# Kernel optimization log

Hardware: AMD Instinct MI355X
Metric: run time of the kernel (lower is better)

The kernel has to match this reference:

```python
import jax, jax.numpy as jnp
import numpy as np

N_NODES = 100000
N_EDGES = 1600000
IN_CH = 128
OUT_CH = 128


def setup_inputs() -> dict:
    key = jax.random.key(0)
    k1, k2, k3 = jax.random.split(key, 3)
    x = jax.random.normal(k1, (N_NODES, IN_CH), dtype=jnp.float32)
    edge_index = jax.random.randint(k2, (2, N_EDGES), 0, N_NODES, dtype=jnp.int64)
    # Glorot-style init like PyG GCNConv
    W = jax.random.normal(k3, (IN_CH, OUT_CH), dtype=jnp.float32) * (1.0 / np.sqrt(IN_CH))
    b = jnp.zeros((OUT_CH,), dtype=jnp.float32)
    return {"x": x, "edge_index": edge_index, "W": W, "b": b}


def reference(x, edge_index, W, b):
    N = x.shape[0]
    # add self-loops (PyG GCNConv default add_self_loops=True)
    loop = jnp.arange(N, dtype=edge_index.dtype)
    src = jnp.concatenate([edge_index[0], loop])
    dst = jnp.concatenate([edge_index[1], loop])
    # symmetric normalization: deg computed over destination (col)
    deg = jax.ops.segment_sum(jnp.ones_like(src, dtype=x.dtype), dst, num_segments=N)
    dinv = jnp.where(deg > 0, jax.lax.rsqrt(deg), 0.0)
    norm = dinv[src] * dinv[dst]  # [E+N]
    xw = x @ W  # [N, out_ch]
    msg = xw[src] * norm[:, None]  # gather + scale, [E+N, out_ch]
    out = jax.ops.segment_sum(msg, dst, num_segments=N) + b  # scatter-add
    return jax.nn.relu(out)
```

## Files before the change

### kernel.cpp

```cpp
#include <hip/hip_runtime.h>
#include <hip/hip_bf16.h>

constexpr int CH    = 128;
constexpr int BSH   = 7;
constexpr int CAPSH = 12;

typedef __attribute__((ext_vector_type(8))) short short8v;
typedef __attribute__((ext_vector_type(4))) float f32x4;

__device__ __forceinline__ unsigned short f2bf(float f) {
    unsigned u = __float_as_uint(f);
    u = (u + 0x7fffu + ((u >> 16) & 1u)) >> 16;
    return (unsigned short)u;
}

__global__ __launch_bounds__(256) void k_bin(const int* __restrict__ src,
                                             const int* __restrict__ dst, int E,
                                             int* __restrict__ bucket_cnt,
                                             unsigned* __restrict__ packed,
                                             const float* __restrict__ W,
                                             unsigned short* __restrict__ Wt,
                                             int nbuck) {
    __shared__ int hist[1024];
    int t = threadIdx.x;
    if (blockIdx.x < 32) {
        int idx = blockIdx.x * 256 + t;
        int c  = idx & 127;
        int k2 = (idx >> 7) * 2;
        unsigned pk = (unsigned)f2bf(W[(size_t)k2 * CH + c]) |
                      ((unsigned)f2bf(W[(size_t)(k2 + 1) * CH + c]) << 16);
        *(unsigned*)(Wt + (size_t)c * CH + k2) = pk;
    }
    for (int i = t; i < nbuck; i += 256) hist[i] = 0;
    __syncthreads();
    int chunk = (E + gridDim.x - 1) / gridDim.x;
    int e0 = blockIdx.x * chunk;
    int e1 = min(e0 + chunk, E);
    for (int e = e0 + t; e < e1; e += 256)
        atomicAdd(&hist[dst[e] >> BSH], 1);
    __syncthreads();
    for (int i = t; i < nbuck; i += 256) {
        int h = hist[i];
        hist[i] = (h > 0) ? atomicAdd(&bucket_cnt[i], h) : 0;
    }
    __syncthreads();
    for (int e = e0 + t; e < e1; e += 256) {
        int d = dst[e];
        int bkt = d >> BSH;
        int pos = atomicAdd(&hist[bkt], 1);
        packed[((size_t)bkt << CAPSH) + pos] =
            (unsigned)src[e] | ((unsigned)(d & ((1 << BSH) - 1)) << 20);
    }
}

__global__ __launch_bounds__(256) void k_bucket(const int* __restrict__ bucket_cnt,
                                                const unsigned* __restrict__ packed,
                                                int* __restrict__ eidx,
                                                uint2* __restrict__ rowinfo,
                                                float* __restrict__ dinv, int N) {
    __shared__ int fh[128];
    __shared__ int fs[128];
    __shared__ int fc[128];
    int b = blockIdx.x;
    int t = threadIdx.x;
    int cnt = bucket_cnt[b];
    if (t < 128) fh[t] = 0;
    __syncthreads();
    const unsigned* pk = packed + ((size_t)b << CAPSH);
    for (int i = t; i < cnt; i += 256)
        atomicAdd(&fh[(pk[i] >> 20) & 127], 1);
    __syncthreads();
    if (t < 128) fs[t] = fh[t];
    __syncthreads();
    for (int off = 1; off < 128; off <<= 1) {
        int v = 0;
        if (t < 128 && t >= off) v = fs[t - off];
        __syncthreads();
        if (t < 128) fs[t] += v;
        __syncthreads();
    }
    if (t < 128) {
        int excl = fs[t] - fh[t];
        fc[t] = excl;
        int node = (b << BSH) + t;
        if (node < N) {
            rowinfo[node] = make_uint2((unsigned)((b << CAPSH) + excl), (unsigned)fh[t]);
            dinv[node] = rsqrtf((float)fh[t] + 1.0f);
        }
    }
    __syncthreads();
    int* eo = eidx + ((size_t)b << CAPSH);
    for (int i = t; i < cnt; i += 256) {
        unsigned p = pk[i];
        int f = (p >> 20) & 127;
        int pos = atomicAdd(&fc[f], 1);
        eo[pos] = (int)(p & 0xFFFFF);
    }
}

__global__ __launch_bounds__(256) void k_gemm(const float* __restrict__ x,
                                              const unsigned short* __restrict__ Wt,
                                              const float* __restrict__ dinv,
                                              unsigned short* __restrict__ xwb, int N) {
    __shared__ __align__(16) unsigned short xs[64 * CH];
    int t = threadIdx.x;
    int w = t >> 6, lane = t & 63;
    int c16 = lane & 15, kq = lane >> 4, kb = kq * 8;
    int row0 = blockIdx.x * 64;
    int arow = row0 + w * 16 + c16;
    bool av = arow < N;
    const float* xp = x + (size_t)(av ? arow : 0) * CH;

    f32x4 acc[8];
    #pragma unroll
    for (int f = 0; f < 8; ++f) acc[f] = (f32x4){0.f, 0.f, 0.f, 0.f};

    #pragma unroll
    for (int kc = 0; kc < 4; ++kc) {
        float4 x0 = make_float4(0.f, 0.f, 0.f, 0.f), x1 = x0;
        if (av) {
            x0 = ((const float4*)(xp + kc * 32 + kb))[0];
            x1 = ((const float4*)(xp + kc * 32 + kb))[1];
        }
        union { short8v v; __hip_bfloat162 h[4]; } au;
        au.h[0] = __float22bfloat162_rn(make_float2(x0.x, x0.y));
        au.h[1] = __float22bfloat162_rn(make_float2(x0.z, x0.w));
        au.h[2] = __float22bfloat162_rn(make_float2(x1.x, x1.y));
        au.h[3] = __float22bfloat162_rn(make_float2(x1.z, x1.w));
        #pragma unroll
        for (int f = 0; f < 8; ++f) {
            short8v b = *(const short8v*)(Wt + (size_t)(f * 16 + c16) * CH + kc * 32 + kb);
            acc[f] = __builtin_amdgcn_mfma_f32_16x16x32_bf16(au.v, b, acc[f], 0, 0, 0);
        }
    }

    #pragma unroll
    for (int r = 0; r < 4; ++r) {
        int row_l = w * 16 + kq * 4 + r;
        int grow  = row0 + row_l;
        float dv  = (grow < N) ? dinv[grow] : 0.f;
        #pragma unroll
        for (int f = 0; f < 8; ++f) {
            int col = f * 16 + c16;
            unsigned bo = ((unsigned)((row_l * CH + col) * 2)) ^ ((unsigned)(row_l & 7) << 4);
            *(unsigned short*)((char*)xs + bo) = f2bf(acc[f][r] * dv);
        }
    }
    __syncthreads();
    #pragma unroll
    for (int i = 0; i < 4; ++i) {
        int g = i * 256 + t;
        int row_l = g >> 4;
        unsigned bo = ((unsigned)(g * 16)) ^ ((unsigned)(row_l & 7) << 4);
        uint4 v = *(const uint4*)((const char*)xs + bo);
        int row = row0 + row_l;
        if (row < N) ((uint4*)(xwb + (size_t)row * CH))[g & 15] = v;
    }
}

__global__ __launch_bounds__(256) void k_gather(const uint2* __restrict__ rowinfo,
                                                const int* __restrict__ eidx,
                                                const unsigned short* __restrict__ xwb,
                                                const float* __restrict__ dinv,
                                                const float* __restrict__ bias,
                                                float* __restrict__ out, int N) {
    int n = blockIdx.x * 4 + (threadIdx.x >> 6);
    if (n >= N) return;
    int lane = threadIdx.x & 63;
    int q    = lane >> 4;
    int c16  = lane & 15;
    uint2 ri = rowinfo[n];
    int beg = (int)ri.x;
    int deg = (int)ri.y;
    float acc[8];
    #pragma unroll
    for (int i = 0; i < 8; ++i) acc[i] = 0.f;

    for (int p0 = 0; p0 < deg; p0 += 64) {
        int m = deg - p0; if (m > 64) m = 64;
        int myi = 0;
        if (lane < m) myi = eidx[beg + p0 + lane];
        for (int j = 0; j < m; j += 4) {
            int jj = j + q;
            int ss = __shfl(myi, jj & 63);
            int s  = (jj < m) ? ss : N;
            uint4 u = ((const uint4*)(xwb + (size_t)s * CH))[c16];
            acc[0] += __uint_as_float(u.x << 16);
            acc[1] += __uint_as_float(u.x & 0xffff0000u);
            acc[2] += __uint_as_float(u.y << 16);
            acc[3] += __uint_as_float(u.y & 0xffff0000u);
            acc[4] += __uint_as_float(u.z << 16);
            acc[5] += __uint_as_float(u.z & 0xffff0000u);
            acc[6] += __uint_as_float(u.w << 16);
            acc[7] += __uint_as_float(u.w & 0xffff0000u);
        }
    }
    #pragma unroll
    for (int i = 0; i < 8; ++i) {
        acc[i] += __shfl_xor(acc[i], 16);
        acc[i] += __shfl_xor(acc[i], 32);
    }
    if (lane < 16) {
        float dn = dinv[n];
        uint4 u = ((const uint4*)(xwb + (size_t)n * CH))[c16];
        acc[0] += __uint_as_float(u.x << 16);
        acc[1] += __uint_as_float(u.x & 0xffff0000u);
        acc[2] += __uint_as_float(u.y << 16);
        acc[3] += __uint_as_float(u.y & 0xffff0000u);
        acc[4] += __uint_as_float(u.z << 16);
        acc[5] += __uint_as_float(u.z & 0xffff0000u);
        acc[6] += __uint_as_float(u.w << 16);
        acc[7] += __uint_as_float(u.w & 0xffff0000u);
        float4 b0 = ((const float4*)bias)[c16 * 2];
        float4 b1 = ((const float4*)bias)[c16 * 2 + 1];
        float4 o0, o1;
        o0.x = fmaxf(fmaf(acc[0], dn, b0.x), 0.f);
        o0.y = fmaxf(fmaf(acc[1], dn, b0.y), 0.f);
        o0.z = fmaxf(fmaf(acc[2], dn, b0.z), 0.f);
        o0.w = fmaxf(fmaf(acc[3], dn, b0.w), 0.f);
        o1.x = fmaxf(fmaf(acc[4], dn, b1.x), 0.f);
        o1.y = fmaxf(fmaf(acc[5], dn, b1.y), 0.f);
        o1.z = fmaxf(fmaf(acc[6], dn, b1.z), 0.f);
        o1.w = fmaxf(fmaf(acc[7], dn, b1.w), 0.f);
        ((float4*)(out + (size_t)n * CH))[c16 * 2]     = o0;
        ((float4*)(out + (size_t)n * CH))[c16 * 2 + 1] = o1;
    }
}

extern "C" void kernel_launch(void* const* d_in, const int* in_sizes, int n_in,
                              void* d_out, int out_size, void* d_ws, size_t ws_size,
                              hipStream_t stream) {
    const float* x  = (const float*)d_in[0];
    const int*   ei = (const int*)d_in[1];
    const float* W  = (const float*)d_in[2];
    const float* b  = (const float*)d_in[3];

    int N = in_sizes[0] / CH;
    int E = in_sizes[1] / 2;
    const int* src = ei;
    const int* dst = ei + E;
    float* out = (float*)d_out;

    int nbuck = (N + (1 << BSH) - 1) >> BSH;
    size_t nslots = (size_t)nbuck << CAPSH;

    auto al = [](uintptr_t p) { return (p + 255) & ~(uintptr_t)255; };
    uintptr_t base = (uintptr_t)d_ws;
    unsigned short* xwb = (unsigned short*)base;
    uintptr_t p = al(base + (size_t)(N + 1) * CH * 2);
    int* bucket_cnt = (int*)p;                 p = al(p + (size_t)nbuck * 4);
    uint2* rowinfo  = (uint2*)p;               p = al(p + (size_t)N * 8);
    float* dinv     = (float*)p;               p = al(p + (size_t)N * 4);
    unsigned short* Wt = (unsigned short*)p;   p = al(p + (size_t)CH * CH * 2);
    unsigned* packed   = (unsigned*)p;         p = al(p + nslots * 4);
    int* eidx          = (int*)p;

    hipMemsetAsync(xwb + (size_t)N * CH, 0, (size_t)CH * 2, stream);
    hipMemsetAsync(bucket_cnt, 0, (size_t)nbuck * 4, stream);
    k_bin   <<<256, 256, 0, stream>>>(src, dst, E, bucket_cnt, packed, W, Wt, nbuck);
    k_bucket<<<nbuck, 256, 0, stream>>>(bucket_cnt, packed, eidx, rowinfo, dinv, N);
    k_gemm  <<<(N + 63) / 64, 256, 0, stream>>>(x, Wt, dinv, xwb, N);
    k_gather<<<(N + 3) / 4, 256, 0, stream>>>(rowinfo, eidx, xwb, dinv, b, out, N);
}
```

Before: 157.9 us.

## Locally sort binned edges in LDS before coalesced scatter; prefetch gather rows

The binning kernel now counting-sorts each block's edge chunk by bucket in shared memory, then writes each bucket's edges to global memory contiguously, replacing scattered single-word writes. This should improve write coalescing into the packed bucket buffer. The gather loop is software-pipelined to issue the next row load before accumulating the current one, and the two memsets are merged into one. The fixed CHUNK size means the block count and the shared-memory capacity of 6400 entries depend on E, and the sort adds a block-wide scan.

Result: faster. 154.4 us (-2.2%).

```diff
diff --git a/kernel.cpp b/kernel.cpp
--- a/kernel.cpp
+++ b/kernel.cpp
@@ -4,6 +4,8 @@
 constexpr int CH    = 128;
 constexpr int BSH   = 7;
 constexpr int CAPSH = 12;
+constexpr int CHUNK = 6250;
+constexpr int CHCAP = 6400;
 
 typedef __attribute__((ext_vector_type(8))) short short8v;
 typedef __attribute__((ext_vector_type(4))) float f32x4;
@@ -19,9 +21,15 @@
                                              int* __restrict__ bucket_cnt,
                                              unsigned* __restrict__ packed,
                                              const float* __restrict__ W,
-                                             unsigned short* __restrict__ Wt,
-                                             int nbuck) {
+                                             unsigned short* __restrict__ Wt) {
     __shared__ int hist[1024];
+    __shared__ int start[1024];
+    __shared__ int cursor[1024];
+    __shared__ int gofs[1024];
+    __shared__ int tscan[256];
+    __shared__ unsigned       sorted[CHCAP];
+    __shared__ unsigned short sbkt[CHCAP];
+
     int t = threadIdx.x;
     if (blockIdx.x < 32) {
         int idx = blockIdx.x * 256 + t;
@@ -31,25 +39,56 @@
                       ((unsigned)f2bf(W[(size_t)(k2 + 1) * CH + c]) << 16);
         *(unsigned*)(Wt + (size_t)c * CH + k2) = pk;
     }
-    for (int i = t; i < nbuck; i += 256) hist[i] = 0;
-    __syncthreads();
-    int chunk = (E + gridDim.x - 1) / gridDim.x;
-    int e0 = blockIdx.x * chunk;
-    int e1 = min(e0 + chunk, E);
+    #pragma unroll
+    for (int i = 0; i < 4; ++i) hist[t + i * 256] = 0;
+    __syncthreads();
+
+    int e0 = blockIdx.x * CHUNK;
+    int e1 = min(e0 + CHUNK, E);
     for (int e = e0 + t; e < e1; e += 256)
         atomicAdd(&hist[dst[e] >> BSH], 1);
     __syncthreads();
-    for (int i = t; i < nbuck; i += 256) {
-        int h = hist[i];
-        hist[i] = (h > 0) ? atomicAdd(&bucket_cnt[i], h) : 0;
+    int b4 = t * 4;
+    int c0 = hist[b4], c1 = hist[b4 + 1], c2 = hist[b4 + 2], c3 = hist[b4 + 3];
+    int tsum = c0 + c1 + c2 + c3;
+    tscan[t] = tsum;
+    __syncthreads();
+    for (int off = 1; off < 256; off <<= 1) {
+        int v = (t >= off) ? tscan[t - off] : 0;
+        __syncthreads();
+        tscan[t] += v;
+        __syncthreads();
+    }
+    int eb = tscan[t] - tsum;
+    start[b4]     = eb;
+    start[b4 + 1] = eb + c0;
+    start[b4 + 2] = eb + c0 + c1;
+    start[b4 + 3] = eb + c0 + c1 + c2;
+    cursor[b4]     = eb;
+    cursor[b4 + 1] = eb + c0;
+    cursor[b4 + 2] = eb + c0 + c1;
+    cursor[b4 + 3] = eb + c0 + c1 + c2;
+    __syncthreads();
+    #pragma unroll
+    for (int i = 0; i < 4; ++i) {
+        int b = t + i * 256;
+        int c = hist[b];
+        gofs[b] = (c > 0) ? atomicAdd(&bucket_cnt[b], c) : 0;
     }
     __syncthreads();
     for (int e = e0 + t; e < e1; e += 256) {
         int d = dst[e];
-        int bkt = d >> BSH;
-        int pos = atomicAdd(&hist[bkt], 1);
-        packed[((size_t)bkt << CAPSH) + pos] =
-            (unsigned)src[e] | ((unsigned)(d & ((1 << BSH) - 1)) << 20);
+        int b = d >> BSH;
+        int pos = atomicAdd(&cursor[b], 1);
+        sorted[pos] = (unsigned)src[e] | ((unsigned)(d & ((1 << BSH) - 1)) << 20);
+        sbkt[pos] = (unsigned short)b;
+    }
+    __syncthreads();
+    int nloc = e1 - e0;
+    for (int i = t; i < nloc; i += 256) {
+        int b = sbkt[i];
+        int gpos = (b << CAPSH) + gofs[b] + (i - start[b]);
+        packed[gpos] = sorted[i];
     }
 }
 
@@ -176,15 +215,19 @@
     #pragma unroll
     for (int i = 0; i < 8; ++i) acc[i] = 0.f;
 
+    const uint4* xw4 = (const uint4*)xwb;
     for (int p0 = 0; p0 < deg; p0 += 64) {
         int m = deg - p0; if (m > 64) m = 64;
         int myi = 0;
         if (lane < m) myi = eidx[beg + p0 + lane];
-        for (int j = 0; j < m; j += 4) {
-            int jj = j + q;
-            int ss = __shfl(myi, jj & 63);
-            int s  = (jj < m) ? ss : N;
-            uint4 u = ((const uint4*)(xwb + (size_t)s * CH))[c16];
+        int jj = q;
+        int s  = (jj < m) ? __shfl(myi, jj & 63) : N;
+        uint4 u = xw4[(size_t)s * 16 + c16];
+        for (int j = 4; j < m; j += 4) {
+            int jj2 = j + q;
+            int ss  = __shfl(myi, jj2 & 63);
+            int s2  = (jj2 < m) ? ss : N;
+            uint4 u2 = xw4[(size_t)s2 * 16 + c16];
             acc[0] += __uint_as_float(u.x << 16);
             acc[1] += __uint_as_float(u.x & 0xffff0000u);
             acc[2] += __uint_as_float(u.y << 16);
@@ -193,7 +236,16 @@
             acc[5] += __uint_as_float(u.z & 0xffff0000u);
             acc[6] += __uint_as_float(u.w << 16);
             acc[7] += __uint_as_float(u.w & 0xffff0000u);
-        }
+            u = u2;
+        }
+        acc[0] += __uint_as_float(u.x << 16);
+        acc[1] += __uint_as_float(u.x & 0xffff0000u);
+        acc[2] += __uint_as_float(u.y << 16);
+        acc[3] += __uint_as_float(u.y & 0xffff0000u);
+        acc[4] += __uint_as_float(u.z << 16);
+        acc[5] += __uint_as_float(u.z & 0xffff0000u);
+        acc[6] += __uint_as_float(u.w << 16);
+        acc[7] += __uint_as_float(u.w & 0xffff0000u);
     }
     #pragma unroll
     for (int i = 0; i < 8; ++i) {
@@ -202,7 +254,7 @@
     }
     if (lane < 16) {
         float dn = dinv[n];
-        uint4 u = ((const uint4*)(xwb + (size_t)n * CH))[c16];
+        uint4 u = xw4[(size_t)n * 16 + c16];
         acc[0] += __uint_as_float(u.x << 16);
         acc[1] += __uint_as_float(u.x & 0xffff0000u);
         acc[2] += __uint_as_float(u.y << 16);
@@ -247,17 +299,18 @@
     auto al = [](uintptr_t p) { return (p + 255) & ~(uintptr_t)255; };
     uintptr_t base = (uintptr_t)d_ws;
     unsigned short* xwb = (unsigned short*)base;
-    uintptr_t p = al(base + (size_t)(N + 1) * CH * 2);
-    int* bucket_cnt = (int*)p;                 p = al(p + (size_t)nbuck * 4);
+    int* bucket_cnt = (int*)(xwb + (size_t)(N + 1) * CH);
+    uintptr_t p = al((uintptr_t)(bucket_cnt + nbuck));
     uint2* rowinfo  = (uint2*)p;               p = al(p + (size_t)N * 8);
     float* dinv     = (float*)p;               p = al(p + (size_t)N * 4);
     unsigned short* Wt = (unsigned short*)p;   p = al(p + (size_t)CH * CH * 2);
     unsigned* packed   = (unsigned*)p;         p = al(p + nslots * 4);
     int* eidx          = (int*)p;
 
-    hipMemsetAsync(xwb + (size_t)N * CH, 0, (size_t)CH * 2, stream);
-    hipMemsetAsync(bucket_cnt, 0, (size_t)nbuck * 4, stream);
-    k_bin   <<<256, 256, 0, stream>>>(src, dst, E, bucket_cnt, packed, W, Wt, nbuck);
+    int nbin = (E + CHUNK - 1) / CHUNK;
+
+    hipMemsetAsync(xwb + (size_t)N * CH, 0, (size_t)CH * 2 + (size_t)nbuck * 4, stream);
+    k_bin   <<<nbin, 256, 0, stream>>>(src, dst, E, bucket_cnt, packed, W, Wt);
     k_bucket<<<nbuck, 256, 0, stream>>>(bucket_cnt, packed, eidx, rowinfo, dinv, N);
     k_gemm  <<<(N + 63) / 64, 256, 0, stream>>>(x, Wt, dinv, xwb, N);
     k_gather<<<(N + 3) / 4, 256, 0, stream>>>(rowinfo, eidx, xwb, dinv, b, out, N);
```
